# Performance work log

Hardware: AMD Instinct MI355X
Metric: run time of the kernel (lower is better)

## Reference

```python
import jax, jax.numpy as jnp
from jax import lax
import numpy as np

B = 8192
NUM_CTX = 300; NUM_STN = 300; NUM_GPE = 20; NUM_GPI = 2; NUM_OUT = 20
FF_DIM = 20; FF_STEPS = 20; STN_ITERS = 50
ETA_GPE = 1.0; ETA_STN = 1.0 / 3.0; ETA_GPI = 0.1
A1 = 1.0; A2 = 1.0; THETAD1 = 0.0; THETAD2 = 0.0
UNITS = (64, 128, 64)

_SPECS = [("vf0", UNITS[0], NUM_CTX), ("vf1", UNITS[1], UNITS[0]), ("vf2", UNITS[2], UNITS[1]), ("vf3", 1, UNITS[2]),
          ("jd1", FF_DIM, NUM_CTX), ("jd2", FF_DIM, NUM_CTX), ("kd1", FF_DIM, NUM_CTX), ("kd2", FF_DIM, NUM_CTX),
          ("sg", NUM_GPE, NUM_STN), ("gs", NUM_STN, NUM_GPE), ("glat", NUM_GPE, NUM_GPE), ("slat", NUM_STN, NUM_STN),
          ("d1gpi", NUM_GPI, FF_DIM), ("stngpi", NUM_GPI, NUM_STN),
          ("ih", 4 * NUM_OUT, NUM_GPI), ("hh", 4 * NUM_OUT, NUM_OUT)]


def _lin_init(k, out_d, in_d):
    kw, kb = jax.random.split(k)
    bound = 1.0 / np.sqrt(in_d)
    w = jax.random.uniform(kw, (out_d, in_d), minval=-bound, maxval=bound, dtype=jnp.float32)
    b = jax.random.uniform(kb, (out_d,), minval=-bound, maxval=bound, dtype=jnp.float32)
    return w, b


def setup_inputs() -> dict:
    key = jax.random.key(0)
    ks = iter(jax.random.split(key, 40))
    inp = {}
    inp["stimulus"] = jax.random.normal(next(ks), (B, NUM_CTX), dtype=jnp.float32)
    inp["deltavf"] = jax.random.normal(next(ks), (B, 1), dtype=jnp.float32)
    inp["hx0"] = jax.random.uniform(next(ks), (B, NUM_OUT), dtype=jnp.float32)
    inp["cx0"] = jax.random.uniform(next(ks), (B, NUM_OUT), dtype=jnp.float32)
    for name, o, i in _SPECS:
        w, b = _lin_init(next(ks), o, i)
        inp["w_" + name] = w
        inp["b_" + name] = b
    return inp


def _lin(x, w, b):
    return x @ w.T + b


def _lstm_cell(x, h, c, w_ih, b_ih, w_hh, b_hh):
    gates = _lin(x, w_ih, b_ih) + _lin(h, w_hh, b_hh)
    i, f, g, o = jnp.split(gates, 4, axis=-1)  # torch LSTMCell gate order
    c_new = jax.nn.sigmoid(f) * c + jax.nn.sigmoid(i) * jnp.tanh(g)
    h_new = jax.nn.sigmoid(o) * jnp.tanh(c_new)
    return h_new, c_new


def reference(stimulus, deltavf, hx0, cx0,
              w_vf0, b_vf0, w_vf1, b_vf1, w_vf2, b_vf2, w_vf3, b_vf3,
              w_jd1, b_jd1, w_jd2, b_jd2, w_kd1, b_kd1, w_kd2, b_kd2,
              w_sg, b_sg, w_gs, b_gs, w_glat, b_glat, w_slat, b_slat,
              w_d1gpi, b_d1gpi, w_stngpi, b_stngpi,
              w_ih, b_ih, w_hh, b_hh):
    bsz = stimulus.shape[0]
    # value function head
    h = jax.nn.relu(_lin(stimulus, w_vf0, b_vf0))
    h = jax.nn.relu(_lin(h, w_vf1, b_vf1))
    h = jax.nn.relu(_lin(h, w_vf2, b_vf2))
    vt = jnp.tanh(_lin(h, w_vf3, b_vf3))  # [B, 1]

    lamd1 = jax.nn.sigmoid(A1 * (deltavf - THETAD1))  # [B, 1]
    lamd2 = jax.nn.sigmoid(A2 * (deltavf - THETAD2))  # [B, 1]

    # loop-invariant striatal drives (computed every iter in torch, same value)
    J_D1 = _lin(stimulus, w_jd1, b_jd1)
    J_D2 = _lin(stimulus, w_jd2, b_jd2)
    K_D1 = _lin(stimulus, w_kd1, b_kd1)
    K_D2 = _lin(stimulus, w_kd2, b_kd2)

    def ff_step(carry, _):
        v1, v2 = carry
        v1 = jax.nn.sigmoid(lamd1 * (J_D1 * (1.0 - v1) + (1.0 - K_D1) * v1))
        v2 = jax.nn.sigmoid(lamd2 * (J_D2 * (1.0 - v2) + (1.0 - K_D2) * v2))
        return (v1, v2), None

    z_ff = jnp.zeros((bsz, FF_DIM), dtype=stimulus.dtype)
    (V_D1, V_D2), _ = lax.scan(ff_step, (z_ff, z_ff), None, length=FF_STEPS)

    V_GPi_DP = _lin(V_D1, w_d1gpi, b_d1gpi)  # [B, num_gpi]

    def stn_step(carry, _):
        xgpe, xstn, vstn, vgpi, hx, cx = carry
        xgpe = xgpe + ETA_GPE * (-xgpe + _lin(vstn, w_sg, b_sg) + _lin(xgpe, w_glat, b_glat) - V_D2)
        xstn = xstn + ETA_STN * (-xstn + _lin(xgpe, w_gs, b_gs) + _lin(vstn, w_slat, b_slat))
        vstn = jnp.tanh(lamd2 * xstn)
        V_GPi_IP = lamd2 * _lin(vstn, w_stngpi, b_stngpi)
        vgpi = vgpi + ETA_GPI * (-vgpi - V_GPi_DP + 2.0 * V_GPi_IP)
        hx, cx = _lstm_cell(-vgpi, hx, cx, w_ih, b_ih, w_hh, b_hh)
        return (xgpe, xstn, vstn, vgpi, hx, cx), None

    carry0 = (jnp.zeros((bsz, NUM_GPE), dtype=stimulus.dtype),
              jnp.zeros((bsz, NUM_STN), dtype=stimulus.dtype),
              jnp.zeros((bsz, NUM_STN), dtype=stimulus.dtype),  # tanh(lamd2*0) = 0
              jnp.zeros((bsz, NUM_GPI), dtype=stimulus.dtype),
              hx0, cx0)
    carry, _ = lax.scan(stn_step, carry0, None, length=STN_ITERS)
    hx = carry[4]
    return hx, vt
```

## Files before the change

### kernel.cpp

```cpp
#include <hip/hip_runtime.h>


typedef _Float16 f16_t;
typedef _Float16 f16x8 __attribute__((ext_vector_type(8)));
typedef _Float16 f16x4 __attribute__((ext_vector_type(4)));
typedef float floatx4 __attribute__((ext_vector_type(4)));

#define BTOT 8192
#define BM   32
#define NTHR 512
#define NBLK 256
#define VSTR 328
#define XST  32

struct Params {
  const float *stimulus, *deltavf, *hx0, *cx0;
  const float *w_vf0, *b_vf0, *w_vf1, *b_vf1, *w_vf2, *b_vf2, *w_vf3, *b_vf3;
  const float *w_jd1, *b_jd1, *w_jd2, *b_jd2, *w_kd1, *b_kd1, *w_kd2, *b_kd2;
  const float *w_sg, *b_sg, *w_gs, *b_gs, *w_glat, *b_glat, *w_slat, *b_slat;
  const float *w_d1gpi, *b_d1gpi, *w_stngpi, *b_stngpi;
  const float *w_ih, *b_ih, *w_hh, *b_hh;
  float* out;
};

struct __align__(16) Smem {
  f16_t vstn[BM * VSTR];
  f16_t xgpe[2][BM * XST];
  f16_t hxf[BM * XST];
  f16_t wB2[21 * 512];
  f16_t wsp[10 * 512];
  f16_t whh[5 * 512];
  union { float h1f[BM * 128]; float scr[3200]; float gates[BM * 80]; } u;
  float h0f[BM * 64];
  float V_D2f[BM * 20];
  float bsumS[304];
  float bsg[20];
  float bihh[80], wih0[80], wih1[80];
  float DPs[BM * 2], vgpis[BM * 2], lamS[BM];
};

__device__ __forceinline__ float rcp_f(float x) { return __builtin_amdgcn_rcpf(x); }
__device__ __forceinline__ float sigm_fast(float x) { return rcp_f(1.f + __expf(-x)); }
__device__ __forceinline__ float tanh_fast(float x) { return 1.f - 2.f * rcp_f(1.f + __expf(2.f * x)); }

__device__ __forceinline__ f16x8 ldfrag(const float* row, int k0, int kmax, bool valid) {
  float4 z = make_float4(0.f, 0.f, 0.f, 0.f);
  int nv = valid ? (kmax - k0) : 0;
  float4 f0 = (nv >= 4) ? *(const float4*)(row + k0) : z;
  float4 f1 = (nv >= 8) ? *(const float4*)(row + k0 + 4) : z;
  f16x8 r;
  r[0] = (f16_t)f0.x; r[1] = (f16_t)f0.y; r[2] = (f16_t)f0.z; r[3] = (f16_t)f0.w;
  r[4] = (f16_t)f1.x; r[5] = (f16_t)f1.y; r[6] = (f16_t)f1.z; r[7] = (f16_t)f1.w;
  return r;
}

__global__ __launch_bounds__(NTHR, 2) void bg_main(Params P) {
  __shared__ Smem S;
  const int tid  = threadIdx.x;
  const int lane = tid & 63;
  const int wv   = tid >> 6;
  const int q    = lane >> 4;
  const int cl   = lane & 15;
  const int row0 = blockIdx.x * BM;
  const floatx4 zf = {0.f, 0.f, 0.f, 0.f};

  if (tid < BM) S.lamS[tid] = sigm_fast(P.deltavf[row0 + tid]);
  for (int i = tid; i < BM * 2; i += NTHR) S.vgpis[i] = 0.f;
  for (int i = tid; i < 2 * BM * XST; i += NTHR) ((f16_t*)S.xgpe)[i] = (f16_t)0.f;
  for (int i = tid; i < BM * XST; i += NTHR) {
    int m = i >> 5, j = i & 31;
    S.hxf[i] = (j < 20) ? (f16_t)P.hx0[row0 * 20 + m * 20 + j] : (f16_t)0.f;
  }
  for (int i = tid; i < BM * VSTR; i += NTHR) S.vstn[i] = (f16_t)0.f;
  for (int i = tid; i < 21 * 512; i += NTHR) {
    int t = i >> 9, l = (i >> 3) & 63, jj = i & 7;
    int c2 = l & 15, k = ((l >> 4) << 3) + jj;
    float v = 0.f;
    if (t < 19) { int n = t * 16 + c2; if (n < 300 && k < 20) v = P.w_gs[n * 20 + k]; }
    else        { int g = (t - 19) * 16 + c2; if (g < 20 && k < 20) v = P.w_glat[g * 20 + k]; }
    S.wB2[i] = (f16_t)v;
  }
  for (int i = tid; i < 10 * 512; i += NTHR) {
    int c = i >> 9, l = (i >> 3) & 63, jj = i & 7;
    int p = l & 15, k = c * 32 + ((l >> 4) << 3) + jj;
    float v = (p < 2 && k < 300) ? P.w_stngpi[p * 300 + k] : 0.f;
    S.wsp[i] = (f16_t)v;
  }
  for (int i = tid; i < 5 * 512; i += NTHR) {
    int t = i >> 9, l = (i >> 3) & 63, jj = i & 7;
    int g = t * 16 + (l & 15), k = ((l >> 4) << 3) + jj;
    S.whh[i] = (f16_t)((k < 20) ? P.w_hh[g * 20 + k] : 0.f);
  }
  for (int i = tid; i < 304; i += NTHR) S.bsumS[i] = (i < 300) ? (P.b_slat[i] + P.b_gs[i]) : 0.f;
  for (int i = tid; i < 20; i += NTHR)  S.bsg[i] = P.b_sg[i] + P.b_glat[i];
  for (int i = tid; i < 80; i += NTHR) {
    S.bihh[i] = P.b_ih[i] + P.b_hh[i];
    S.wih0[i] = P.w_ih[i * 2 + 0];
    S.wih1[i] = P.w_ih[i * 2 + 1];
  }

  {
    int o = tid & 63, mb = (tid >> 6) * 4;
    const float4* wr = (const float4*)(P.w_vf0 + o * 300);
    float bias = P.b_vf0[o], a[4];
#pragma unroll
    for (int u = 0; u < 4; ++u) a[u] = bias;
    for (int kq = 0; kq < 75; ++kq) {
      float4 w = wr[kq];
#pragma unroll
      for (int u = 0; u < 4; ++u) {
        float4 v = *(const float4*)(P.stimulus + (size_t)(row0 + mb + u) * 300 + kq * 4);
        a[u] = fmaf(v.x, w.x, a[u]); a[u] = fmaf(v.y, w.y, a[u]);
        a[u] = fmaf(v.z, w.z, a[u]); a[u] = fmaf(v.w, w.w, a[u]);
      }
    }
#pragma unroll
    for (int u = 0; u < 4; ++u) S.h0f[(mb + u) * 64 + o] = fmaxf(a[u], 0.f);
  }
  __syncthreads();
  {
    int o = tid & 127, mb = (tid >> 7) * 8;
    const float* wr = P.w_vf1 + o * 64;
    float bias = P.b_vf1[o], a[8];
#pragma unroll
    for (int u = 0; u < 8; ++u) a[u] = bias;
    for (int k = 0; k < 64; ++k) {
      float w = wr[k];
#pragma unroll
      for (int u = 0; u < 8; ++u) a[u] = fmaf(S.h0f[(mb + u) * 64 + k], w, a[u]);
    }
#pragma unroll
    for (int u = 0; u < 8; ++u) S.u.h1f[(mb + u) * 128 + o] = fmaxf(a[u], 0.f);
  }
  __syncthreads();
  {
    int o = tid & 63, mb = (tid >> 6) * 4;
    const float* wr = P.w_vf2 + o * 128;
    float bias = P.b_vf2[o], a[4];
#pragma unroll
    for (int u = 0; u < 4; ++u) a[u] = bias;
    for (int k = 0; k < 128; ++k) {
      float w = wr[k];
#pragma unroll
      for (int u = 0; u < 4; ++u) a[u] = fmaf(S.u.h1f[(mb + u) * 128 + k], w, a[u]);
    }
#pragma unroll
    for (int u = 0; u < 4; ++u) S.h0f[(mb + u) * 64 + o] = fmaxf(a[u], 0.f);
  }
  __syncthreads();
  {
    int oid = tid & 127, mb = (tid >> 7) * 8;
    if (oid < 80) {
      int which = oid / 20, o = oid - which * 20;
      const float *wp, *bp;
      if (which == 0)      { wp = P.w_jd1; bp = P.b_jd1; }
      else if (which == 1) { wp = P.w_jd2; bp = P.b_jd2; }
      else if (which == 2) { wp = P.w_kd1; bp = P.b_kd1; }
      else                 { wp = P.w_kd2; bp = P.b_kd2; }
      float bias = bp[o], a[8];
#pragma unroll
      for (int u = 0; u < 8; ++u) a[u] = bias;
      for (int kq = 0; kq < 75; ++kq) {
        float4 w = *(const float4*)(wp + o * 300 + kq * 4);
#pragma unroll
        for (int u = 0; u < 8; ++u) {
          float4 v = *(const float4*)(P.stimulus + (size_t)(row0 + mb + u) * 300 + kq * 4);
          a[u] = fmaf(v.x, w.x, a[u]); a[u] = fmaf(v.y, w.y, a[u]);
          a[u] = fmaf(v.z, w.z, a[u]); a[u] = fmaf(v.w, w.w, a[u]);
        }
      }
#pragma unroll
      for (int u = 0; u < 8; ++u) S.u.scr[which * 640 + (mb + u) * 20 + o] = a[u];
    }
    if (tid < BM) {
      float a = P.b_vf3[0];
      for (int k = 0; k < 64; ++k) a = fmaf(S.h0f[tid * 64 + k], P.w_vf3[k], a);
      P.out[(size_t)BTOT * 20 + row0 + tid] = tanh_fast(a);
    }
  }
  __syncthreads();
  for (int i = tid; i < BM * 20; i += NTHR) {
    int m = i / 20;
    float j1 = S.u.scr[i],        j2 = S.u.scr[640 + i];
    float k1 = S.u.scr[1280 + i], k2 = S.u.scr[1920 + i];
    float L = S.lamS[m], v1 = 0.f, v2 = 0.f;
    for (int s = 0; s < 20; ++s) {
      v1 = sigm_fast(L * (j1 * (1.f - v1) + (1.f - k1) * v1));
      v2 = sigm_fast(L * (j2 * (1.f - v2) + (1.f - k2) * v2));
    }
    S.u.scr[2560 + i] = v1;
    S.V_D2f[i] = v2;
  }
  __syncthreads();
  if (tid < BM * 2) {
    int m = tid >> 1, p2 = tid & 1;
    float a = P.b_d1gpi[p2];
    for (int o = 0; o < 20; ++o) a = fmaf(S.u.scr[2560 + m * 20 + o], P.w_d1gpi[p2 * 20 + o], a);
    S.DPs[tid] = a;
  }
  __syncthreads();

  f16x8 Ws[3][10];
#pragma unroll
  for (int j = 0; j < 3; ++j) {
    int t = wv + 8 * j;
    if (t < 19) {
      int n = t * 16 + cl;
#pragma unroll
      for (int c = 0; c < 10; ++c)
        Ws[j][c] = ldfrag(P.w_slat + (size_t)(n < 300 ? n : 0) * 300, c * 32 + q * 8, 300, n < 300);
    } else if (t < 21) {
      int g = (t - 19) * 16 + cl;
#pragma unroll
      for (int c = 0; c < 10; ++c)
        Ws[j][c] = ldfrag(P.w_sg + (size_t)(g < 20 ? g : 0) * 300, c * 32 + q * 8, 300, g < 20);
    } else {
      f16x8 z;
#pragma unroll
      for (int e = 0; e < 8; ++e) z[e] = (f16_t)0.f;
#pragma unroll
      for (int c = 0; c < 10; ++c) Ws[j][c] = z;
    }
  }
  const float lam0 = S.lamS[cl], lam1 = S.lamS[cl + 16];
  const float bstn0 = P.b_stngpi[0], bstn1 = P.b_stngpi[1];
  const int e0 = tid,        m0 = e0 / 20, j0 = e0 - m0 * 20;
  const int e1 = tid + NTHR, m1 = e1 / 20, j1 = e1 - m1 * 20;
  const bool hase1 = (tid < BM * 20 - NTHR);
  float cxr0 = P.cx0[row0 * 20 + e0], hxr0 = P.hx0[row0 * 20 + e0];
  float cxr1 = hase1 ? P.cx0[row0 * 20 + e1] : 0.f;
  float hxr1 = hase1 ? P.hx0[row0 * 20 + e1] : 0.f;

  float xs[3][2][4];
#pragma unroll
  for (int j = 0; j < 3; ++j)
#pragma unroll
    for (int mf = 0; mf < 2; ++mf)
#pragma unroll
      for (int r = 0; r < 4; ++r) xs[j][mf][r] = 0.f;

  for (int it = 0; it < 50; ++it) {
    const int po = it & 1, pn = po ^ 1;
    floatx4 acc[3][2];
#pragma unroll
    for (int j = 0; j < 3; ++j) { acc[j][0] = zf; acc[j][1] = zf; }

#pragma unroll
    for (int c = 0; c < 10; ++c) {
      f16x8 b0 = *(const f16x8*)&S.vstn[cl * VSTR + c * 32 + q * 8];
      f16x8 b1 = *(const f16x8*)&S.vstn[(16 + cl) * VSTR + c * 32 + q * 8];
#pragma unroll
      for (int j = 0; j < 3; ++j) {
        if (wv + 8 * j < 21) {
          acc[j][0] = __builtin_amdgcn_mfma_f32_16x16x32_f16(Ws[j][c], b0, acc[j][0], 0, 0, 0);
          acc[j][1] = __builtin_amdgcn_mfma_f32_16x16x32_f16(Ws[j][c], b1, acc[j][1], 0, 0, 0);
        }
      }
    }
    if (wv == 3 || wv == 4) {
      f16x8 Wg = *(const f16x8*)&S.wB2[(wv + 16) * 512 + lane * 8];
      f16x8 g0 = *(const f16x8*)&S.xgpe[po][cl * XST + q * 8];
      f16x8 g1 = *(const f16x8*)&S.xgpe[po][(16 + cl) * XST + q * 8];
      acc[2][0] = __builtin_amdgcn_mfma_f32_16x16x32_f16(Wg, g0, acc[2][0], 0, 0, 0);
      acc[2][1] = __builtin_amdgcn_mfma_f32_16x16x32_f16(Wg, g1, acc[2][1], 0, 0, 0);
      int g0i = (wv - 3) * 16 + q * 4;
      if (g0i < 20) {
        floatx4 bg4 = *(const floatx4*)&S.bsg[g0i];
#pragma unroll
        for (int mf = 0; mf < 2; ++mf) {
          int batch = cl + 16 * mf;
          floatx4 vd4 = *(const floatx4*)&S.V_D2f[batch * 20 + g0i];
          f16x4 pk;
#pragma unroll
          for (int r = 0; r < 4; ++r) pk[r] = (f16_t)(acc[2][mf][r] + bg4[r] - vd4[r]);
          *(f16x4*)&S.xgpe[pn][batch * XST + g0i] = pk;
        }
      }
    }
    __syncthreads();

    {
      f16x8 x0 = *(const f16x8*)&S.xgpe[pn][cl * XST + q * 8];
      f16x8 x1 = *(const f16x8*)&S.xgpe[pn][(16 + cl) * XST + q * 8];
#pragma unroll
      for (int j = 0; j < 3; ++j) {
        int t = wv + 8 * j;
        if (t < 19) {
          f16x8 Wg = *(const f16x8*)&S.wB2[t * 512 + lane * 8];
          acc[j][0] = __builtin_amdgcn_mfma_f32_16x16x32_f16(Wg, x0, acc[j][0], 0, 0, 0);
          acc[j][1] = __builtin_amdgcn_mfma_f32_16x16x32_f16(Wg, x1, acc[j][1], 0, 0, 0);
        }
      }
#pragma unroll
      for (int j = 0; j < 3; ++j) {
        int t = wv + 8 * j;
        if (t < 19) {
          int n0 = t * 16 + q * 4;
          if (!(t == 18 && q == 3)) {
            floatx4 bs4 = *(const floatx4*)&S.bsumS[n0];
#pragma unroll
            for (int mf = 0; mf < 2; ++mf) {
              float lm = mf ? lam1 : lam0;
              f16x4 pk;
#pragma unroll
              for (int r = 0; r < 4; ++r) {
                float xo = xs[j][mf][r];
                float xn = xo + (1.0f / 3.0f) * (acc[j][mf][r] + bs4[r] - xo);
                xs[j][mf][r] = xn;
                pk[r] = (f16_t)tanh_fast(lm * xn);
              }
              *(f16x4*)&S.vstn[(cl + 16 * mf) * VSTR + n0] = pk;
            }
          }
        }
      }
    }
    __syncthreads();

    if (wv == 5) {
      floatx4 ip0 = zf, ip1 = zf;
#pragma unroll
      for (int c = 0; c < 10; ++c) {
        f16x8 Wp = *(const f16x8*)&S.wsp[c * 512 + lane * 8];
        f16x8 b0 = *(const f16x8*)&S.vstn[cl * VSTR + c * 32 + q * 8];
        f16x8 b1 = *(const f16x8*)&S.vstn[(16 + cl) * VSTR + c * 32 + q * 8];
        ip0 = __builtin_amdgcn_mfma_f32_16x16x32_f16(Wp, b0, ip0, 0, 0, 0);
        ip1 = __builtin_amdgcn_mfma_f32_16x16x32_f16(Wp, b1, ip1, 0, 0, 0);
      }
      if (q == 0) {
#pragma unroll
        for (int mf = 0; mf < 2; ++mf) {
          int batch = cl + 16 * mf;
          float lm = mf ? lam1 : lam0;
#pragma unroll
          for (int p = 0; p < 2; ++p) {
            float raw = (mf ? ip1[p] : ip0[p]) + (p ? bstn1 : bstn0);
            float ipv = lm * raw;
            int idx = batch * 2 + p;
            float v = S.vgpis[idx];
            v = v + 0.1f * (-v - S.DPs[idx] + 2.f * ipv);
            S.vgpis[idx] = v;
          }
        }
      }
    } else if (wv < 5) {
      f16x8 Wh = *(const f16x8*)&S.whh[wv * 512 + lane * 8];
      f16x8 h0 = *(const f16x8*)&S.hxf[cl * XST + q * 8];
      f16x8 h1 = *(const f16x8*)&S.hxf[(16 + cl) * XST + q * 8];
      floatx4 gA = __builtin_amdgcn_mfma_f32_16x16x32_f16(Wh, h0, zf, 0, 0, 0);
      floatx4 gB = __builtin_amdgcn_mfma_f32_16x16x32_f16(Wh, h1, zf, 0, 0, 0);
      int gb = wv * 16 + q * 4;
      *(floatx4*)&S.u.gates[cl * 80 + gb] = gA;
      *(floatx4*)&S.u.gates[(cl + 16) * 80 + gb] = gB;
    }
    __syncthreads();

    {
      float v0 = S.vgpis[m0 * 2], v1 = S.vgpis[m0 * 2 + 1];
      float gi = S.u.gates[m0 * 80 + j0]      + S.bihh[j0]      - S.wih0[j0] * v0      - S.wih1[j0] * v1;
      float gf = S.u.gates[m0 * 80 + 20 + j0] + S.bihh[20 + j0] - S.wih0[20 + j0] * v0 - S.wih1[20 + j0] * v1;
      float gg = S.u.gates[m0 * 80 + 40 + j0] + S.bihh[40 + j0] - S.wih0[40 + j0] * v0 - S.wih1[40 + j0] * v1;
      float go = S.u.gates[m0 * 80 + 60 + j0] + S.bihh[60 + j0] - S.wih0[60 + j0] * v0 - S.wih1[60 + j0] * v1;
      float cn = sigm_fast(gf) * cxr0 + sigm_fast(gi) * tanh_fast(gg);
      cxr0 = cn;
      hxr0 = sigm_fast(go) * tanh_fast(cn);
      S.hxf[m0 * XST + j0] = (f16_t)hxr0;
    }
    if (hase1) {
      float v0 = S.vgpis[m1 * 2], v1 = S.vgpis[m1 * 2 + 1];
      float gi = S.u.gates[m1 * 80 + j1]      + S.bihh[j1]      - S.wih0[j1] * v0      - S.wih1[j1] * v1;
      float gf = S.u.gates[m1 * 80 + 20 + j1] + S.bihh[20 + j1] - S.wih0[20 + j1] * v0 - S.wih1[20 + j1] * v1;
      float gg = S.u.gates[m1 * 80 + 40 + j1] + S.bihh[40 + j1] - S.wih0[40 + j1] * v0 - S.wih1[40 + j1] * v1;
      float go = S.u.gates[m1 * 80 + 60 + j1] + S.bihh[60 + j1] - S.wih0[60 + j1] * v0 - S.wih1[60 + j1] * v1;
      float cn = sigm_fast(gf) * cxr1 + sigm_fast(gi) * tanh_fast(gg);
      cxr1 = cn;
      hxr1 = sigm_fast(go) * tanh_fast(cn);
      S.hxf[m1 * XST + j1] = (f16_t)hxr1;
    }
    __syncthreads();
  }

  P.out[(size_t)row0 * 20 + e0] = hxr0;
  if (hase1) P.out[(size_t)row0 * 20 + e1] = hxr1;
}

extern "C" void kernel_launch(void* const* d_in, const int* in_sizes, int n_in,
                              void* d_out, int out_size, void* d_ws, size_t ws_size,
                              hipStream_t stream) {
  (void)in_sizes; (void)n_in; (void)out_size; (void)d_ws; (void)ws_size;
  Params P;
  P.stimulus = (const float*)d_in[0];
  P.deltavf  = (const float*)d_in[1];
  P.hx0 = (const float*)d_in[2];
  P.cx0 = (const float*)d_in[3];
  P.w_vf0 = (const float*)d_in[4];  P.b_vf0 = (const float*)d_in[5];
  P.w_vf1 = (const float*)d_in[6];  P.b_vf1 = (const float*)d_in[7];
  P.w_vf2 = (const float*)d_in[8];  P.b_vf2 = (const float*)d_in[9];
  P.w_vf3 = (const float*)d_in[10]; P.b_vf3 = (const float*)d_in[11];
  P.w_jd1 = (const float*)d_in[12]; P.b_jd1 = (const float*)d_in[13];
  P.w_jd2 = (const float*)d_in[14]; P.b_jd2 = (const float*)d_in[15];
  P.w_kd1 = (const float*)d_in[16]; P.b_kd1 = (const float*)d_in[17];
  P.w_kd2 = (const float*)d_in[18]; P.b_kd2 = (const float*)d_in[19];
  P.w_sg  = (const float*)d_in[20]; P.b_sg  = (const float*)d_in[21];
  P.w_gs  = (const float*)d_in[22]; P.b_gs  = (const float*)d_in[23];
  P.w_glat= (const float*)d_in[24]; P.b_glat= (const float*)d_in[25];
  P.w_slat= (const float*)d_in[26]; P.b_slat= (const float*)d_in[27];
  P.w_d1gpi  = (const float*)d_in[28]; P.b_d1gpi  = (const float*)d_in[29];
  P.w_stngpi = (const float*)d_in[30]; P.b_stngpi = (const float*)d_in[31];
  P.w_ih = (const float*)d_in[32]; P.b_ih = (const float*)d_in[33];
  P.w_hh = (const float*)d_in[34]; P.b_hh = (const float*)d_in[35];
  P.out  = (float*)d_out;
  bg_main<<<NBLK, NTHR, 0, stream>>>(P);
}
```

Baseline: 416.1 us.

## Widen block to 12 waves, rebalance STN tiles, drop per-iteration barrier

Raises the block from 8 to 12 waves and gives each wave at most two STN/GPe output tiles instead of three. The recurrent-gate MFMAs move into the same phase as the xgpe contributions, and the STN→GPi product is split across three waves with partial sums kept in shared memory. GPi state now lives in registers, each LSTM thread owns one element, and the trailing barrier per iteration is removed. This aims to shorten the serial critical path of each of the 50 iterations, at the cost of higher register pressure under the 3-blocks-per-CU launch bound and idle threads in the MLP prologue.

```diff
diff --git a/kernel.cpp b/kernel.cpp
--- a/kernel.cpp
+++ b/kernel.cpp
@@ -5,10 +5,11 @@
 typedef _Float16 f16x8 __attribute__((ext_vector_type(8)));
 typedef _Float16 f16x4 __attribute__((ext_vector_type(4)));
 typedef float floatx4 __attribute__((ext_vector_type(4)));
+typedef float floatx2 __attribute__((ext_vector_type(2)));
 
 #define BTOT 8192
 #define BM   32
-#define NTHR 512
+#define NTHR 768
 #define NBLK 256
 #define VSTR 328
 #define XST  32
@@ -33,10 +34,11 @@
   union { float h1f[BM * 128]; float scr[3200]; float gates[BM * 80]; } u;
   float h0f[BM * 64];
   float V_D2f[BM * 20];
+  float pp[3][64];
   float bsumS[304];
   float bsg[20];
   float bihh[80], wih0[80], wih1[80];
-  float DPs[BM * 2], vgpis[BM * 2], lamS[BM];
+  float DPs[BM * 2], lamS[BM];
 };
 
 __device__ __forceinline__ float rcp_f(float x) { return __builtin_amdgcn_rcpf(x); }
@@ -54,7 +56,7 @@
   return r;
 }
 
-__global__ __launch_bounds__(NTHR, 2) void bg_main(Params P) {
+__global__ __launch_bounds__(NTHR, 3) void bg_main(Params P) {
   __shared__ Smem S;
   const int tid  = threadIdx.x;
   const int lane = tid & 63;
@@ -64,8 +66,14 @@
   const int row0 = blockIdx.x * BM;
   const floatx4 zf = {0.f, 0.f, 0.f, 0.f};
 
+  const int  t0s  = wv;
+  const int  t1s  = (wv < 7) ? (12 + wv) : (wv == 7 ? 19 : (wv == 8 ? 20 : 255));
+  const bool has1 = (t1s != 255);
+  const bool isSg = (t1s == 19 || t1s == 20);
+  const bool gs1  = (t1s < 19);
+  const int  gtile = (wv >= 9) ? (wv - 9) : (wv == 7 ? 3 : (wv == 8 ? 4 : -1));
+
   if (tid < BM) S.lamS[tid] = sigm_fast(P.deltavf[row0 + tid]);
-  for (int i = tid; i < BM * 2; i += NTHR) S.vgpis[i] = 0.f;
   for (int i = tid; i < 2 * BM * XST; i += NTHR) ((f16_t*)S.xgpe)[i] = (f16_t)0.f;
   for (int i = tid; i < BM * XST; i += NTHR) {
     int m = i >> 5, j = i & 31;
@@ -99,7 +107,7 @@
     S.wih1[i] = P.w_ih[i * 2 + 1];
   }
 
-  {
+  if (tid < 512) {
     int o = tid & 63, mb = (tid >> 6) * 4;
     const float4* wr = (const float4*)(P.w_vf0 + o * 300);
     float bias = P.b_vf0[o], a[4];
@@ -118,7 +126,7 @@
     for (int u = 0; u < 4; ++u) S.h0f[(mb + u) * 64 + o] = fmaxf(a[u], 0.f);
   }
   __syncthreads();
-  {
+  if (tid < 512) {
     int o = tid & 127, mb = (tid >> 7) * 8;
     const float* wr = P.w_vf1 + o * 64;
     float bias = P.b_vf1[o], a[8];
@@ -133,7 +141,7 @@
     for (int u = 0; u < 8; ++u) S.u.h1f[(mb + u) * 128 + o] = fmaxf(a[u], 0.f);
   }
   __syncthreads();
-  {
+  if (tid < 512) {
     int o = tid & 63, mb = (tid >> 6) * 4;
     const float* wr = P.w_vf2 + o * 128;
     float bias = P.b_vf2[o], a[4];
@@ -150,7 +158,7 @@
   __syncthreads();
   {
     int oid = tid & 127, mb = (tid >> 7) * 8;
-    if (oid < 80) {
+    if (tid < 512 && oid < 80) {
       int which = oid / 20, o = oid - which * 20;
       const float *wp, *bp;
       if (which == 0)      { wp = P.w_jd1; bp = P.b_jd1; }
@@ -200,40 +208,45 @@
   }
   __syncthreads();
 
-  f16x8 Ws[3][10];
-#pragma unroll
-  for (int j = 0; j < 3; ++j) {
-    int t = wv + 8 * j;
-    if (t < 19) {
-      int n = t * 16 + cl;
-#pragma unroll
-      for (int c = 0; c < 10; ++c)
-        Ws[j][c] = ldfrag(P.w_slat + (size_t)(n < 300 ? n : 0) * 300, c * 32 + q * 8, 300, n < 300);
-    } else if (t < 21) {
-      int g = (t - 19) * 16 + cl;
-#pragma unroll
-      for (int c = 0; c < 10; ++c)
-        Ws[j][c] = ldfrag(P.w_sg + (size_t)(g < 20 ? g : 0) * 300, c * 32 + q * 8, 300, g < 20);
+  const float lam0 = S.lamS[cl], lam1 = S.lamS[cl + 16];
+  const float bstn0 = P.b_stngpi[0], bstn1 = P.b_stngpi[1];
+  const bool lown = (tid < BM * 20);
+  const int  m0 = lown ? tid / 20 : 0;
+  const int  j0 = tid - m0 * 20;
+  const float lamr = S.lamS[m0];
+  const float DP0 = S.DPs[m0 * 2], DP1 = S.DPs[m0 * 2 + 1];
+  float cxr0 = lown ? P.cx0[row0 * 20 + tid] : 0.f;
+  float hxr0 = 0.f;
+  float vg0 = 0.f, vg1 = 0.f;
+
+  f16x8 Ws[2][10];
+  {
+    int n = t0s * 16 + cl;
+    const float* a0 = P.w_slat + (size_t)n * 300;
+#pragma unroll
+    for (int c = 0; c < 10; ++c) Ws[0][c] = ldfrag(a0, c * 32 + q * 8, 300, true);
+    if (t1s < 19) {
+      int n1 = t1s * 16 + cl;
+      const float* a1 = P.w_slat + (size_t)(n1 < 300 ? n1 : 0) * 300;
+#pragma unroll
+      for (int c = 0; c < 10; ++c) Ws[1][c] = ldfrag(a1, c * 32 + q * 8, 300, n1 < 300);
+    } else if (isSg) {
+      int g = (t1s - 19) * 16 + cl;
+      const float* a1 = P.w_sg + (size_t)(g < 20 ? g : 0) * 300;
+#pragma unroll
+      for (int c = 0; c < 10; ++c) Ws[1][c] = ldfrag(a1, c * 32 + q * 8, 300, g < 20);
     } else {
       f16x8 z;
 #pragma unroll
       for (int e = 0; e < 8; ++e) z[e] = (f16_t)0.f;
 #pragma unroll
-      for (int c = 0; c < 10; ++c) Ws[j][c] = z;
-    }
-  }
-  const float lam0 = S.lamS[cl], lam1 = S.lamS[cl + 16];
-  const float bstn0 = P.b_stngpi[0], bstn1 = P.b_stngpi[1];
-  const int e0 = tid,        m0 = e0 / 20, j0 = e0 - m0 * 20;
-  const int e1 = tid + NTHR, m1 = e1 / 20, j1 = e1 - m1 * 20;
-  const bool hase1 = (tid < BM * 20 - NTHR);
-  float cxr0 = P.cx0[row0 * 20 + e0], hxr0 = P.hx0[row0 * 20 + e0];
-  float cxr1 = hase1 ? P.cx0[row0 * 20 + e1] : 0.f;
-  float hxr1 = hase1 ? P.hx0[row0 * 20 + e1] : 0.f;
-
-  float xs[3][2][4];
-#pragma unroll
-  for (int j = 0; j < 3; ++j)
+      for (int c = 0; c < 10; ++c) Ws[1][c] = z;
+    }
+  }
+
+  float xs[2][2][4];
+#pragma unroll
+  for (int j = 0; j < 2; ++j)
 #pragma unroll
     for (int mf = 0; mf < 2; ++mf)
 #pragma unroll
@@ -241,29 +254,37 @@
 
   for (int it = 0; it < 50; ++it) {
     const int po = it & 1, pn = po ^ 1;
-    floatx4 acc[3][2];
-#pragma unroll
-    for (int j = 0; j < 3; ++j) { acc[j][0] = zf; acc[j][1] = zf; }
-
-#pragma unroll
-    for (int c = 0; c < 10; ++c) {
-      f16x8 b0 = *(const f16x8*)&S.vstn[cl * VSTR + c * 32 + q * 8];
-      f16x8 b1 = *(const f16x8*)&S.vstn[(16 + cl) * VSTR + c * 32 + q * 8];
-#pragma unroll
-      for (int j = 0; j < 3; ++j) {
-        if (wv + 8 * j < 21) {
-          acc[j][0] = __builtin_amdgcn_mfma_f32_16x16x32_f16(Ws[j][c], b0, acc[j][0], 0, 0, 0);
-          acc[j][1] = __builtin_amdgcn_mfma_f32_16x16x32_f16(Ws[j][c], b1, acc[j][1], 0, 0, 0);
-        }
-      }
-    }
-    if (wv == 3 || wv == 4) {
-      f16x8 Wg = *(const f16x8*)&S.wB2[(wv + 16) * 512 + lane * 8];
+    floatx4 acc[2][2];
+    acc[0][0] = zf; acc[0][1] = zf; acc[1][0] = zf; acc[1][1] = zf;
+
+    __builtin_amdgcn_s_setprio(1);
+    if (has1) {
+#pragma unroll
+      for (int c = 0; c < 10; ++c) {
+        f16x8 b0 = *(const f16x8*)&S.vstn[cl * VSTR + c * 32 + q * 8];
+        f16x8 b1 = *(const f16x8*)&S.vstn[(16 + cl) * VSTR + c * 32 + q * 8];
+        acc[0][0] = __builtin_amdgcn_mfma_f32_16x16x32_f16(Ws[0][c], b0, acc[0][0], 0, 0, 0);
+        acc[0][1] = __builtin_amdgcn_mfma_f32_16x16x32_f16(Ws[0][c], b1, acc[0][1], 0, 0, 0);
+        acc[1][0] = __builtin_amdgcn_mfma_f32_16x16x32_f16(Ws[1][c], b0, acc[1][0], 0, 0, 0);
+        acc[1][1] = __builtin_amdgcn_mfma_f32_16x16x32_f16(Ws[1][c], b1, acc[1][1], 0, 0, 0);
+      }
+    } else {
+#pragma unroll
+      for (int c = 0; c < 10; ++c) {
+        f16x8 b0 = *(const f16x8*)&S.vstn[cl * VSTR + c * 32 + q * 8];
+        f16x8 b1 = *(const f16x8*)&S.vstn[(16 + cl) * VSTR + c * 32 + q * 8];
+        acc[0][0] = __builtin_amdgcn_mfma_f32_16x16x32_f16(Ws[0][c], b0, acc[0][0], 0, 0, 0);
+        acc[0][1] = __builtin_amdgcn_mfma_f32_16x16x32_f16(Ws[0][c], b1, acc[0][1], 0, 0, 0);
+      }
+    }
+    __builtin_amdgcn_s_setprio(0);
+    if (isSg) {
+      f16x8 Wg = *(const f16x8*)&S.wB2[t1s * 512 + lane * 8];
       f16x8 g0 = *(const f16x8*)&S.xgpe[po][cl * XST + q * 8];
       f16x8 g1 = *(const f16x8*)&S.xgpe[po][(16 + cl) * XST + q * 8];
-      acc[2][0] = __builtin_amdgcn_mfma_f32_16x16x32_f16(Wg, g0, acc[2][0], 0, 0, 0);
-      acc[2][1] = __builtin_amdgcn_mfma_f32_16x16x32_f16(Wg, g1, acc[2][1], 0, 0, 0);
-      int g0i = (wv - 3) * 16 + q * 4;
+      acc[1][0] = __builtin_amdgcn_mfma_f32_16x16x32_f16(Wg, g0, acc[1][0], 0, 0, 0);
+      acc[1][1] = __builtin_amdgcn_mfma_f32_16x16x32_f16(Wg, g1, acc[1][1], 0, 0, 0);
+      int g0i = (t1s - 19) * 16 + q * 4;
       if (g0i < 20) {
         floatx4 bg4 = *(const floatx4*)&S.bsg[g0i];
 #pragma unroll
@@ -272,7 +293,7 @@
           floatx4 vd4 = *(const floatx4*)&S.V_D2f[batch * 20 + g0i];
           f16x4 pk;
 #pragma unroll
-          for (int r = 0; r < 4; ++r) pk[r] = (f16_t)(acc[2][mf][r] + bg4[r] - vd4[r]);
+          for (int r = 0; r < 4; ++r) pk[r] = (f16_t)(acc[1][mf][r] + bg4[r] - vd4[r]);
           *(f16x4*)&S.xgpe[pn][batch * XST + g0i] = pk;
         }
       }
@@ -282,18 +303,29 @@
     {
       f16x8 x0 = *(const f16x8*)&S.xgpe[pn][cl * XST + q * 8];
       f16x8 x1 = *(const f16x8*)&S.xgpe[pn][(16 + cl) * XST + q * 8];
-#pragma unroll
-      for (int j = 0; j < 3; ++j) {
-        int t = wv + 8 * j;
-        if (t < 19) {
-          f16x8 Wg = *(const f16x8*)&S.wB2[t * 512 + lane * 8];
-          acc[j][0] = __builtin_amdgcn_mfma_f32_16x16x32_f16(Wg, x0, acc[j][0], 0, 0, 0);
-          acc[j][1] = __builtin_amdgcn_mfma_f32_16x16x32_f16(Wg, x1, acc[j][1], 0, 0, 0);
-        }
-      }
-#pragma unroll
-      for (int j = 0; j < 3; ++j) {
-        int t = wv + 8 * j;
+      {
+        f16x8 Wg0 = *(const f16x8*)&S.wB2[t0s * 512 + lane * 8];
+        acc[0][0] = __builtin_amdgcn_mfma_f32_16x16x32_f16(Wg0, x0, acc[0][0], 0, 0, 0);
+        acc[0][1] = __builtin_amdgcn_mfma_f32_16x16x32_f16(Wg0, x1, acc[0][1], 0, 0, 0);
+      }
+      if (gs1) {
+        f16x8 Wg1 = *(const f16x8*)&S.wB2[t1s * 512 + lane * 8];
+        acc[1][0] = __builtin_amdgcn_mfma_f32_16x16x32_f16(Wg1, x0, acc[1][0], 0, 0, 0);
+        acc[1][1] = __builtin_amdgcn_mfma_f32_16x16x32_f16(Wg1, x1, acc[1][1], 0, 0, 0);
+      }
+      if (gtile >= 0) {
+        f16x8 Wh = *(const f16x8*)&S.whh[gtile * 512 + lane * 8];
+        f16x8 h0 = *(const f16x8*)&S.hxf[cl * XST + q * 8];
+        f16x8 h1 = *(const f16x8*)&S.hxf[(16 + cl) * XST + q * 8];
+        floatx4 gA = __builtin_amdgcn_mfma_f32_16x16x32_f16(Wh, h0, zf, 0, 0, 0);
+        floatx4 gB = __builtin_amdgcn_mfma_f32_16x16x32_f16(Wh, h1, zf, 0, 0, 0);
+        int gb = gtile * 16 + q * 4;
+        *(floatx4*)&S.u.gates[cl * 80 + gb] = gA;
+        *(floatx4*)&S.u.gates[(cl + 16) * 80 + gb] = gB;
+      }
+#pragma unroll
+      for (int j = 0; j < 2; ++j) {
+        int t = j ? t1s : t0s;
         if (t < 19) {
           int n0 = t * 16 + q * 4;
           if (!(t == 18 && q == 3)) {
@@ -317,10 +349,11 @@
     }
     __syncthreads();
 
-    if (wv == 5) {
+    if (wv >= 9) {
+      const int c0 = (wv == 9) ? 0 : (wv == 10 ? 4 : 7);
+      const int c1 = (wv == 9) ? 4 : (wv == 10 ? 7 : 10);
       floatx4 ip0 = zf, ip1 = zf;
-#pragma unroll
-      for (int c = 0; c < 10; ++c) {
+      for (int c = c0; c < c1; ++c) {
         f16x8 Wp = *(const f16x8*)&S.wsp[c * 512 + lane * 8];
         f16x8 b0 = *(const f16x8*)&S.vstn[cl * VSTR + c * 32 + q * 8];
         f16x8 b1 = *(const f16x8*)&S.vstn[(16 + cl) * VSTR + c * 32 + q * 8];
@@ -328,60 +361,33 @@
         ip1 = __builtin_amdgcn_mfma_f32_16x16x32_f16(Wp, b1, ip1, 0, 0, 0);
       }
       if (q == 0) {
-#pragma unroll
-        for (int mf = 0; mf < 2; ++mf) {
-          int batch = cl + 16 * mf;
-          float lm = mf ? lam1 : lam0;
-#pragma unroll
-          for (int p = 0; p < 2; ++p) {
-            float raw = (mf ? ip1[p] : ip0[p]) + (p ? bstn1 : bstn0);
-            float ipv = lm * raw;
-            int idx = batch * 2 + p;
-            float v = S.vgpis[idx];
-            v = v + 0.1f * (-v - S.DPs[idx] + 2.f * ipv);
-            S.vgpis[idx] = v;
-          }
-        }
-      }
-    } else if (wv < 5) {
-      f16x8 Wh = *(const f16x8*)&S.whh[wv * 512 + lane * 8];
-      f16x8 h0 = *(const f16x8*)&S.hxf[cl * XST + q * 8];
-      f16x8 h1 = *(const f16x8*)&S.hxf[(16 + cl) * XST + q * 8];
-      floatx4 gA = __builtin_amdgcn_mfma_f32_16x16x32_f16(Wh, h0, zf, 0, 0, 0);
-      floatx4 gB = __builtin_amdgcn_mfma_f32_16x16x32_f16(Wh, h1, zf, 0, 0, 0);
-      int gb = wv * 16 + q * 4;
-      *(floatx4*)&S.u.gates[cl * 80 + gb] = gA;
-      *(floatx4*)&S.u.gates[(cl + 16) * 80 + gb] = gB;
+        floatx2 w0; w0[0] = ip0[0]; w0[1] = ip0[1];
+        floatx2 w1; w1[0] = ip1[0]; w1[1] = ip1[1];
+        *(floatx2*)&S.pp[wv - 9][cl * 2] = w0;
+        *(floatx2*)&S.pp[wv - 9][(16 + cl) * 2] = w1;
+      }
     }
     __syncthreads();
 
-    {
-      float v0 = S.vgpis[m0 * 2], v1 = S.vgpis[m0 * 2 + 1];
-      float gi = S.u.gates[m0 * 80 + j0]      + S.bihh[j0]      - S.wih0[j0] * v0      - S.wih1[j0] * v1;
-      float gf = S.u.gates[m0 * 80 + 20 + j0] + S.bihh[20 + j0] - S.wih0[20 + j0] * v0 - S.wih1[20 + j0] * v1;
-      float gg = S.u.gates[m0 * 80 + 40 + j0] + S.bihh[40 + j0] - S.wih0[40 + j0] * v0 - S.wih1[40 + j0] * v1;
-      float go = S.u.gates[m0 * 80 + 60 + j0] + S.bihh[60 + j0] - S.wih0[60 + j0] * v0 - S.wih1[60 + j0] * v1;
+    if (lown) {
+      float s0 = S.pp[0][m0 * 2]     + S.pp[1][m0 * 2]     + S.pp[2][m0 * 2];
+      float s1 = S.pp[0][m0 * 2 + 1] + S.pp[1][m0 * 2 + 1] + S.pp[2][m0 * 2 + 1];
+      float ipa = lamr * (s0 + bstn0);
+      float ipb = lamr * (s1 + bstn1);
+      vg0 = vg0 + 0.1f * (-vg0 - DP0 + 2.f * ipa);
+      vg1 = vg1 + 0.1f * (-vg1 - DP1 + 2.f * ipb);
+      float gi = S.u.gates[m0 * 80 + j0]      + S.bihh[j0]      - S.wih0[j0] * vg0      - S.wih1[j0] * vg1;
+      float gf = S.u.gates[m0 * 80 + 20 + j0] + S.bihh[20 + j0] - S.wih0[20 + j0] * vg0 - S.wih1[20 + j0] * vg1;
+      float gg = S.u.gates[m0 * 80 + 40 + j0] + S.bihh[40 + j0] - S.wih0[40 + j0] * vg0 - S.wih1[40 + j0] * vg1;
+      float go = S.u.gates[m0 * 80 + 60 + j0] + S.bihh[60 + j0] - S.wih0[60 + j0] * vg0 - S.wih1[60 + j0] * vg1;
       float cn = sigm_fast(gf) * cxr0 + sigm_fast(gi) * tanh_fast(gg);
       cxr0 = cn;
       hxr0 = sigm_fast(go) * tanh_fast(cn);
       S.hxf[m0 * XST + j0] = (f16_t)hxr0;
     }
-    if (hase1) {
-      float v0 = S.vgpis[m1 * 2], v1 = S.vgpis[m1 * 2 + 1];
-      float gi = S.u.gates[m1 * 80 + j1]      + S.bihh[j1]      - S.wih0[j1] * v0      - S.wih1[j1] * v1;
-      float gf = S.u.gates[m1 * 80 + 20 + j1] + S.bihh[20 + j1] - S.wih0[20 + j1] * v0 - S.wih1[20 + j1] * v1;
-      float gg = S.u.gates[m1 * 80 + 40 + j1] + S.bihh[40 + j1] - S.wih0[40 + j1] * v0 - S.wih1[40 + j1] * v1;
-      float go = S.u.gates[m1 * 80 + 60 + j1] + S.bihh[60 + j1] - S.wih0[60 + j1] * v0 - S.wih1[60 + j1] * v1;
-      float cn = sigm_fast(gf) * cxr1 + sigm_fast(gi) * tanh_fast(gg);
-      cxr1 = cn;
-      hxr1 = sigm_fast(go) * tanh_fast(cn);
-      S.hxf[m1 * XST + j1] = (f16_t)hxr1;
-    }
-    __syncthreads();
-  }
-
-  P.out[(size_t)row0 * 20 + e0] = hxr0;
-  if (hase1) P.out[(size_t)row0 * 20 + e1] = hxr1;
+  }
+
+  if (lown) P.out[(size_t)row0 * 20 + tid] = hxr0;
 }
 
 extern "C" void kernel_launch(void* const* d_in, const int* in_sizes, int n_in,
```

Measured after the change: 406.1 us. 1.02x faster.

## Drop per-iteration barrier, fold STN state into MFMA accumulators, vectorize LSTM gates

Applied to the files above, without the earlier changes.

The recurrent-weight gate MFMA moves into the second phase so one __syncthreads per STN iteration can be removed; the double-buffered and phased shared-memory state still keeps the ordering safe. The STN state now lives in the MFMA accumulators, seeded with 2/3 of the previous value, so the separate xs registers and the per-iteration zeroing go away. The w_hh rows are permuted so each LSTM thread reads its four gates, biases and input weights with vector loads, and the main MFMA loop runs at raised wave priority. The risks are a subtle ordering dependency after the barrier is gone and a changed rounding order in the state update.

```diff
diff --git a/kernel.cpp b/kernel.cpp
--- a/kernel.cpp
+++ b/kernel.cpp
@@ -5,6 +5,7 @@
 typedef _Float16 f16x8 __attribute__((ext_vector_type(8)));
 typedef _Float16 f16x4 __attribute__((ext_vector_type(4)));
 typedef float floatx4 __attribute__((ext_vector_type(4)));
+typedef float floatx2 __attribute__((ext_vector_type(2)));
 
 #define BTOT 8192
 #define BM   32
@@ -33,9 +34,9 @@
   union { float h1f[BM * 128]; float scr[3200]; float gates[BM * 80]; } u;
   float h0f[BM * 64];
   float V_D2f[BM * 20];
+  float lstmc[20][12];
   float bsumS[304];
   float bsg[20];
-  float bihh[80], wih0[80], wih1[80];
   float DPs[BM * 2], vgpis[BM * 2], lamS[BM];
 };
 
@@ -88,16 +89,20 @@
   }
   for (int i = tid; i < 5 * 512; i += NTHR) {
     int t = i >> 9, l = (i >> 3) & 63, jj = i & 7;
-    int g = t * 16 + (l & 15), k = ((l >> 4) << 3) + jj;
-    S.whh[i] = (f16_t)((k < 20) ? P.w_hh[g * 20 + k] : 0.f);
+    int c2 = l & 15, k = ((l >> 4) << 3) + jj;
+    int orig = (c2 & 3) * 20 + 4 * t + (c2 >> 2);
+    S.whh[i] = (f16_t)((k < 20) ? P.w_hh[orig * 20 + k] : 0.f);
+  }
+  for (int i = tid; i < 240; i += NTHR) {
+    int j = i / 12, c = i - j * 12;
+    float v;
+    if (c < 4)      v = P.b_ih[c * 20 + j] + P.b_hh[c * 20 + j];
+    else if (c < 8) v = P.w_ih[((c - 4) * 20 + j) * 2 + 0];
+    else            v = P.w_ih[((c - 8) * 20 + j) * 2 + 1];
+    S.lstmc[j][c] = v;
   }
   for (int i = tid; i < 304; i += NTHR) S.bsumS[i] = (i < 300) ? (P.b_slat[i] + P.b_gs[i]) : 0.f;
   for (int i = tid; i < 20; i += NTHR)  S.bsg[i] = P.b_sg[i] + P.b_glat[i];
-  for (int i = tid; i < 80; i += NTHR) {
-    S.bihh[i] = P.b_ih[i] + P.b_hh[i];
-    S.wih0[i] = P.w_ih[i * 2 + 0];
-    S.wih1[i] = P.w_ih[i * 2 + 1];
-  }
 
   {
     int o = tid & 63, mb = (tid >> 6) * 4;
@@ -230,21 +235,17 @@
   float cxr0 = P.cx0[row0 * 20 + e0], hxr0 = P.hx0[row0 * 20 + e0];
   float cxr1 = hase1 ? P.cx0[row0 * 20 + e1] : 0.f;
   float hxr1 = hase1 ? P.hx0[row0 * 20 + e1] : 0.f;
-
-  float xs[3][2][4];
-#pragma unroll
-  for (int j = 0; j < 3; ++j)
-#pragma unroll
-    for (int mf = 0; mf < 2; ++mf)
-#pragma unroll
-      for (int r = 0; r < 4; ++r) xs[j][mf][r] = 0.f;
+  const bool isSgW = (wv == 3 || wv == 4);
+
+  floatx4 acc[3][2];
+#pragma unroll
+  for (int j = 0; j < 3; ++j) { acc[j][0] = zf; acc[j][1] = zf; }
 
   for (int it = 0; it < 50; ++it) {
     const int po = it & 1, pn = po ^ 1;
-    floatx4 acc[3][2];
-#pragma unroll
-    for (int j = 0; j < 3; ++j) { acc[j][0] = zf; acc[j][1] = zf; }
-
+    if (isSgW) { acc[2][0] = zf; acc[2][1] = zf; }
+
+    __builtin_amdgcn_s_setprio(1);
 #pragma unroll
     for (int c = 0; c < 10; ++c) {
       f16x8 b0 = *(const f16x8*)&S.vstn[cl * VSTR + c * 32 + q * 8];
@@ -257,7 +258,8 @@
         }
       }
     }
-    if (wv == 3 || wv == 4) {
+    __builtin_amdgcn_s_setprio(0);
+    if (isSgW) {
       f16x8 Wg = *(const f16x8*)&S.wB2[(wv + 16) * 512 + lane * 8];
       f16x8 g0 = *(const f16x8*)&S.xgpe[po][cl * XST + q * 8];
       f16x8 g1 = *(const f16x8*)&S.xgpe[po][(16 + cl) * XST + q * 8];
@@ -282,6 +284,16 @@
     {
       f16x8 x0 = *(const f16x8*)&S.xgpe[pn][cl * XST + q * 8];
       f16x8 x1 = *(const f16x8*)&S.xgpe[pn][(16 + cl) * XST + q * 8];
+      if (wv < 5) {
+        f16x8 Wh = *(const f16x8*)&S.whh[wv * 512 + lane * 8];
+        f16x8 h0 = *(const f16x8*)&S.hxf[cl * XST + q * 8];
+        f16x8 h1 = *(const f16x8*)&S.hxf[(16 + cl) * XST + q * 8];
+        floatx4 gA = __builtin_amdgcn_mfma_f32_16x16x32_f16(Wh, h0, zf, 0, 0, 0);
+        floatx4 gB = __builtin_amdgcn_mfma_f32_16x16x32_f16(Wh, h1, zf, 0, 0, 0);
+        int gb = wv * 16 + q * 4;
+        *(floatx4*)&S.u.gates[cl * 80 + gb] = gA;
+        *(floatx4*)&S.u.gates[(cl + 16) * 80 + gb] = gB;
+      }
 #pragma unroll
       for (int j = 0; j < 3; ++j) {
         int t = wv + 8 * j;
@@ -304,9 +316,9 @@
               f16x4 pk;
 #pragma unroll
               for (int r = 0; r < 4; ++r) {
-                float xo = xs[j][mf][r];
-                float xn = xo + (1.0f / 3.0f) * (acc[j][mf][r] + bs4[r] - xo);
-                xs[j][mf][r] = xn;
+                float tmp = acc[j][mf][r] + bs4[r];
+                float xn  = tmp * (1.0f / 3.0f);
+                acc[j][mf][r] = tmp * (2.0f / 3.0f);
                 pk[r] = (f16_t)tanh_fast(lm * xn);
               }
               *(f16x4*)&S.vstn[(cl + 16 * mf) * VSTR + n0] = pk;
@@ -332,52 +344,48 @@
         for (int mf = 0; mf < 2; ++mf) {
           int batch = cl + 16 * mf;
           float lm = mf ? lam1 : lam0;
-#pragma unroll
-          for (int p = 0; p < 2; ++p) {
-            float raw = (mf ? ip1[p] : ip0[p]) + (p ? bstn1 : bstn0);
-            float ipv = lm * raw;
-            int idx = batch * 2 + p;
-            float v = S.vgpis[idx];
-            v = v + 0.1f * (-v - S.DPs[idx] + 2.f * ipv);
-            S.vgpis[idx] = v;
-          }
-        }
-      }
-    } else if (wv < 5) {
-      f16x8 Wh = *(const f16x8*)&S.whh[wv * 512 + lane * 8];
-      f16x8 h0 = *(const f16x8*)&S.hxf[cl * XST + q * 8];
-      f16x8 h1 = *(const f16x8*)&S.hxf[(16 + cl) * XST + q * 8];
-      floatx4 gA = __builtin_amdgcn_mfma_f32_16x16x32_f16(Wh, h0, zf, 0, 0, 0);
-      floatx4 gB = __builtin_amdgcn_mfma_f32_16x16x32_f16(Wh, h1, zf, 0, 0, 0);
-      int gb = wv * 16 + q * 4;
-      *(floatx4*)&S.u.gates[cl * 80 + gb] = gA;
-      *(floatx4*)&S.u.gates[(cl + 16) * 80 + gb] = gB;
+          floatx2 vg = *(const floatx2*)&S.vgpis[batch * 2];
+          floatx2 dp = *(const floatx2*)&S.DPs[batch * 2];
+          float ipa = lm * ((mf ? ip1[0] : ip0[0]) + bstn0);
+          float ipb = lm * ((mf ? ip1[1] : ip0[1]) + bstn1);
+          vg[0] = vg[0] + 0.1f * (-vg[0] - dp[0] + 2.f * ipa);
+          vg[1] = vg[1] + 0.1f * (-vg[1] - dp[1] + 2.f * ipb);
+          *(floatx2*)&S.vgpis[batch * 2] = vg;
+        }
+      }
     }
     __syncthreads();
 
     {
-      float v0 = S.vgpis[m0 * 2], v1 = S.vgpis[m0 * 2 + 1];
-      float gi = S.u.gates[m0 * 80 + j0]      + S.bihh[j0]      - S.wih0[j0] * v0      - S.wih1[j0] * v1;
-      float gf = S.u.gates[m0 * 80 + 20 + j0] + S.bihh[20 + j0] - S.wih0[20 + j0] * v0 - S.wih1[20 + j0] * v1;
-      float gg = S.u.gates[m0 * 80 + 40 + j0] + S.bihh[40 + j0] - S.wih0[40 + j0] * v0 - S.wih1[40 + j0] * v1;
-      float go = S.u.gates[m0 * 80 + 60 + j0] + S.bihh[60 + j0] - S.wih0[60 + j0] * v0 - S.wih1[60 + j0] * v1;
+      floatx4 g4 = *(const floatx4*)&S.u.gates[m0 * 80 + j0 * 4];
+      floatx4 cb = *(const floatx4*)&S.lstmc[j0][0];
+      floatx4 w0 = *(const floatx4*)&S.lstmc[j0][4];
+      floatx4 w1 = *(const floatx4*)&S.lstmc[j0][8];
+      floatx2 vg = *(const floatx2*)&S.vgpis[m0 * 2];
+      float gi = g4[0] + cb[0] - w0[0] * vg[0] - w1[0] * vg[1];
+      float gf = g4[1] + cb[1] - w0[1] * vg[0] - w1[1] * vg[1];
+      float gg = g4[2] + cb[2] - w0[2] * vg[0] - w1[2] * vg[1];
+      float go = g4[3] + cb[3] - w0[3] * vg[0] - w1[3] * vg[1];
       float cn = sigm_fast(gf) * cxr0 + sigm_fast(gi) * tanh_fast(gg);
       cxr0 = cn;
       hxr0 = sigm_fast(go) * tanh_fast(cn);
       S.hxf[m0 * XST + j0] = (f16_t)hxr0;
     }
     if (hase1) {
-      float v0 = S.vgpis[m1 * 2], v1 = S.vgpis[m1 * 2 + 1];
-      float gi = S.u.gates[m1 * 80 + j1]      + S.bihh[j1]      - S.wih0[j1] * v0      - S.wih1[j1] * v1;
-      float gf = S.u.gates[m1 * 80 + 20 + j1] + S.bihh[20 + j1] - S.wih0[20 + j1] * v0 - S.wih1[20 + j1] * v1;
-      float gg = S.u.gates[m1 * 80 + 40 + j1] + S.bihh[40 + j1] - S.wih0[40 + j1] * v0 - S.wih1[40 + j1] * v1;
-      float go = S.u.gates[m1 * 80 + 60 + j1] + S.bihh[60 + j1] - S.wih0[60 + j1] * v0 - S.wih1[60 + j1] * v1;
+      floatx4 g4 = *(const floatx4*)&S.u.gates[m1 * 80 + j1 * 4];
+      floatx4 cb = *(const floatx4*)&S.lstmc[j1][0];
+      floatx4 w0 = *(const floatx4*)&S.lstmc[j1][4];
+      floatx4 w1 = *(const floatx4*)&S.lstmc[j1][8];
+      floatx2 vg = *(const floatx2*)&S.vgpis[m1 * 2];
+      float gi = g4[0] + cb[0] - w0[0] * vg[0] - w1[0] * vg[1];
+      float gf = g4[1] + cb[1] - w0[1] * vg[0] - w1[1] * vg[1];
+      float gg = g4[2] + cb[2] - w0[2] * vg[0] - w1[2] * vg[1];
+      float go = g4[3] + cb[3] - w0[3] * vg[0] - w1[3] * vg[1];
       float cn = sigm_fast(gf) * cxr1 + sigm_fast(gi) * tanh_fast(gg);
       cxr1 = cn;
       hxr1 = sigm_fast(go) * tanh_fast(cn);
       S.hxf[m1 * XST + j1] = (f16_t)hxr1;
     }
-    __syncthreads();
   }
 
   P.out[(size_t)row0 * 20 + e0] = hxr0;
```

Measured after the change: 408.2 us. Within noise of the previous version (-1.9%).
